# Optimization experiments

Hardware: AMD Instinct MI355X
Metric: run time of the kernel (lower is better)

The kernel has to match this reference:

```python
import jax, jax.numpy as jnp
import numpy as np

NM, ND = 50000, 50000          # mirna / disease node counts
DM, DD = 256, 256              # m_sim / d_sim feature dims
F = 64                         # feature_attn_size
E = 1600000                    # number of edges (avg degree 16)
N = NM + ND
SLOPE = 0.2                    # leaky_relu negative slope


def setup_inputs() -> dict:
    key = jax.random.key(0)
    k1, k2, k3, k4, k5, k6 = jax.random.split(key, 6)
    return {
        "m_sim": jax.random.normal(k1, (NM, DM), dtype=jnp.float32),
        "d_sim": jax.random.normal(k2, (ND, DD), dtype=jnp.float32),
        "Wm": jax.random.normal(k3, (F, DM), dtype=jnp.float32) / np.sqrt(DM).astype(np.float32),
        "Wd": jax.random.normal(k4, (F, DD), dtype=jnp.float32) / np.sqrt(DD).astype(np.float32),
        "src": jax.random.randint(k5, (E,), 0, N),
        "dst": jax.random.randint(k6, (E,), 0, N),
    }


def reference(m_sim, d_sim, Wm, Wd, src, dst):
    # node projection (dropout omitted: eval mode). mirna nodes first, then disease nodes.
    z = jnp.concatenate([m_sim @ Wm.T, d_sim @ Wd.T], axis=0)  # [N, F]

    # edge attention score: dot(z_src, z_dst) then leaky_relu
    z_src = z[src]                                             # [E, F] gather
    e = jnp.sum(z_src * z[dst], axis=1)                        # [E]
    e = jax.nn.leaky_relu(e, SLOPE)

    # segment softmax over incoming edges of each dst node (numerically stable)
    emax = jax.ops.segment_max(e, dst, num_segments=N)         # [N]
    emax = jnp.where(jnp.isfinite(emax), emax, 0.0)            # isolated nodes
    ex = jnp.exp(e - emax[dst])                                # [E]
    denom = jax.ops.segment_sum(ex, dst, num_segments=N)       # [N]
    alpha = ex / denom[dst]                                    # [E]

    # weighted aggregation + elu (isolated nodes get h=0, elu(0)=0)
    h = jax.ops.segment_sum(alpha[:, None] * z_src, dst, num_segments=N)  # [N, F]
    return jax.nn.elu(h)
```

## Files before the change

### kernel.cpp

```cpp
#include <hip/hip_runtime.h>
#include <math.h>

#define NM 50000
#define ND 50000
#define NN 100000
#define DK 256
#define F  64
#define SLOPE 0.2f

#define NBZ   391
#define NPROJ (NBZ * 2)

#define NBUCK 391
#define BCAP  8192
#define CH    4096

typedef short bf16x8 __attribute__((ext_vector_type(8)));
typedef float f32x4  __attribute__((ext_vector_type(4)));

__device__ __forceinline__ void cvt8(const float4& a0, const float4& a1,
                                     bf16x8& hi, bf16x8& lo) {
    float v[8] = {a0.x, a0.y, a0.z, a0.w, a1.x, a1.y, a1.z, a1.w};
    #pragma unroll
    for (int e = 0; e < 8; ++e) {
        unsigned u  = __float_as_uint(v[e]);
        unsigned r  = u + 0x7FFF + ((u >> 16) & 1);
        unsigned short hb = (unsigned short)(r >> 16);
        float hf = __uint_as_float(((unsigned)hb) << 16);
        float lf = v[e] - hf;
        unsigned ul = __float_as_uint(lf);
        unsigned rl = ul + 0x7FFF + ((ul >> 16) & 1);
        hi[e] = (short)hb;
        lo[e] = (short)(rl >> 16);
    }
}

__global__ __launch_bounds__(512, 1) void fused1(const float* __restrict__ m_sim,
                                                 const float* __restrict__ d_sim,
                                                 const float* __restrict__ Wm,
                                                 const float* __restrict__ Wd,
                                                 float* __restrict__ z,
                                                 const int* __restrict__ src,
                                                 const int* __restrict__ dst,
                                                 int* __restrict__ pkb_g,
                                                 int* __restrict__ bcur,
                                                 int nchunks, int E) {
    __shared__ __align__(16) char smem[65536];
    int t = threadIdx.x;

    if ((int)blockIdx.x < nchunks) {
        int* cnt   = (int*)smem;
        int* scx   = cnt + 512;
        int* lcur  = scx + 512;
        int* gbase = lcur + 512;
        int* pkb_l = gbase + 512;
        int* bkt_l = pkb_l + CH;

        int base = blockIdx.x * CH;
        int chunkN = E - base; if (chunkN > CH) chunkN = CH;

        cnt[t] = 0;
        __syncthreads();

        int ss[8], ds[8];
        #pragma unroll
        for (int e = 0; e < 8; ++e) {
            int k = base + e * 512 + t;
            if (e * 512 + t < chunkN) {
                ds[e] = dst[k];
                ss[e] = src[k];
                atomicAdd(&cnt[ds[e] >> 8], 1);
            }
        }
        __syncthreads();

        int x = cnt[t];
        scx[t] = x;
        __syncthreads();
        for (int off = 1; off < 512; off <<= 1) {
            int v = (t >= off) ? scx[t - off] : 0;
            __syncthreads();
            scx[t] += v;
            __syncthreads();
        }
        int lexcl = scx[t] - x;
        scx[t] = lexcl;
        lcur[t] = lexcl;
        gbase[t] = atomicAdd(&bcur[t], x);
        __syncthreads();

        #pragma unroll
        for (int e = 0; e < 8; ++e) {
            if (e * 512 + t < chunkN) {
                int b = ds[e] >> 8;
                int p = atomicAdd(&lcur[b], 1);
                pkb_l[p] = (ss[e] << 8) | (ds[e] & 255);
                bkt_l[p] = b;
            }
        }
        __syncthreads();

        for (int idx = t; idx < chunkN; idx += 512) {
            int b = bkt_l[idx];
            int g = b * BCAP + gbase[b] + (idx - scx[b]);
            pkb_g[g] = pkb_l[idx];
        }
        return;
    }

    short* Whi = (short*)smem;
    short* Wlo = (short*)(smem + 32768);

    int bid  = blockIdx.x - nchunks;
    bool ism = bid < NBZ;
    const float* sim = ism ? m_sim : d_sim;
    const float* W   = ism ? Wm : Wd;
    int row0   = (ism ? bid : bid - NBZ) * 128;
    int nrows  = ism ? NM : ND;
    int zbase  = ism ? 0 : NM;

    int l = t & 63;
    int w = t >> 6;
    int frow = l & 15;
    int kg   = l >> 4;

    int grow = row0 + w * 16 + frow; if (grow > nrows - 1) grow = nrows - 1;
    const float4* ap = (const float4*)(sim + (size_t)grow * DK) + kg * 2;

    float4 pa0 = ap[0], pa1 = ap[1];
    float4 pb0 = ap[8], pb1 = ap[9];

    {
        int r = t >> 3;
        int q = t & 7;
        const float4* wr = (const float4*)(W + (size_t)r * DK);
        #pragma unroll
        for (int i = 0; i < 4; ++i) {
            int ls = q * 4 + i;
            float4 b0 = wr[ls * 2], b1 = wr[ls * 2 + 1];
            bf16x8 hi, lo;
            cvt8(b0, b1, hi, lo);
            int ps = ls ^ (r & 7);
            *(bf16x8*)&Whi[r * 256 + ps * 8] = hi;
            *(bf16x8*)&Wlo[r * 256 + ps * 8] = lo;
        }
    }
    __syncthreads();

    f32x4 acc[4];
    #pragma unroll
    for (int j = 0; j < 4; ++j) acc[j] = (f32x4){0.f, 0.f, 0.f, 0.f};

    #pragma unroll 1
    for (int step = 0; step < 8; ++step) {
        bf16x8 ahi, alo;
        cvt8(pa0, pa1, ahi, alo);
        pa0 = pb0; pa1 = pb1;
        if (step + 2 < 8) {
            pb0 = ap[(step + 2) * 8];
            pb1 = ap[(step + 2) * 8 + 1];
        }

        int ls = step * 4 + kg;
        #pragma unroll
        for (int j = 0; j < 4; ++j) {
            int wrow = j * 16 + frow;
            int ps = ls ^ (wrow & 7);
            bf16x8 bhi = *(const bf16x8*)&Whi[wrow * 256 + ps * 8];
            bf16x8 blo = *(const bf16x8*)&Wlo[wrow * 256 + ps * 8];
            acc[j] = __builtin_amdgcn_mfma_f32_16x16x32_bf16(ahi, bhi, acc[j], 0, 0, 0);
            acc[j] = __builtin_amdgcn_mfma_f32_16x16x32_bf16(ahi, blo, acc[j], 0, 0, 0);
            acc[j] = __builtin_amdgcn_mfma_f32_16x16x32_bf16(alo, bhi, acc[j], 0, 0, 0);
        }
    }

    #pragma unroll
    for (int j = 0; j < 4; ++j) {
        #pragma unroll
        for (int reg = 0; reg < 4; ++reg) {
            int r = row0 + w * 16 + kg * 4 + reg;
            if (r < nrows)
                z[(size_t)(zbase + r) * F + j * 16 + frow] = acc[j][reg];
        }
    }
}

__global__ __launch_bounds__(512) void scanBuck(const int* __restrict__ bcur,
                                                int* __restrict__ bbase) {
    __shared__ int sd[512];
    int t = threadIdx.x;
    int x = (t < NBUCK) ? bcur[t] : 0;
    sd[t] = x;
    __syncthreads();
    for (int off = 1; off < 512; off <<= 1) {
        int v = (t >= off) ? sd[t - off] : 0;
        __syncthreads();
        sd[t] += v;
        __syncthreads();
    }
    if (t < NBUCK) bbase[t] = sd[t] - x;
}

__global__ __launch_bounds__(256) void scatter3(const int* __restrict__ pkb_g,
                                                const int* __restrict__ bcur,
                                                const int* __restrict__ bbase,
                                                int* __restrict__ offs,
                                                int* __restrict__ csr) {
    __shared__ int dcnt[256], loc[256], lcur[256];
    int b = blockIdx.x;
    int t = threadIdx.x;
    int node0 = b << 8;
    int nbe  = bcur[b];
    int base = bbase[b];
    const int* pp = pkb_g + (size_t)b * BCAP;

    dcnt[t] = 0;
    __syncthreads();
    for (int i = t; i < nbe; i += 256)
        atomicAdd(&dcnt[pp[i] & 255], 1);
    __syncthreads();

    int x = dcnt[t];
    loc[t] = x;
    __syncthreads();
    for (int off = 1; off < 256; off <<= 1) {
        int v = (t >= off) ? loc[t - off] : 0;
        __syncthreads();
        loc[t] += v;
        __syncthreads();
    }
    int excl = loc[t] - x;
    int node = node0 + t;
    if (node < NN) offs[node] = base + excl;
    if (b == NBUCK - 1 && t == 0) offs[NN] = base + nbe;
    lcur[t] = base + excl;
    __syncthreads();

    for (int i = t; i < nbe; i += 256) {
        int pk = pp[i];
        int pos = atomicAdd(&lcur[pk & 255], 1);
        csr[pos] = pk >> 8;
    }
}

__global__ __launch_bounds__(256) void gat_kernel(const float* __restrict__ z,
                                                  const int* __restrict__ offs,
                                                  const int* __restrict__ csr_src,
                                                  float* __restrict__ out) {
    int tid  = threadIdx.x;
    int node = blockIdx.x * 4 + (tid >> 6);
    int lane = tid & 63;
    int g    = lane >> 4;
    int i    = lane & 15;
    int beg = offs[node];
    int end = offs[node + 1];

    float4 zd = *(const float4*)&z[(size_t)node * F + i * 4];

    float  m = -1e30f, ssum = 0.f;
    float4 h = {0.f, 0.f, 0.f, 0.f};

    for (int j = beg; j < end; j += 16) {
        int   idx[4];
        bool  val[4];
        float4 v[4];
        float p[4], e[4], ex[4];
        #pragma unroll
        for (int k = 0; k < 4; ++k) {
            int jj = j + k * 4 + g;
            val[k] = jj < end;
            idx[k] = csr_src[val[k] ? jj : beg];
        }
        #pragma unroll
        for (int k = 0; k < 4; ++k)
            v[k] = *(const float4*)&z[(size_t)idx[k] * F + i * 4];
        #pragma unroll
        for (int k = 0; k < 4; ++k)
            p[k] = v[k].x * zd.x + v[k].y * zd.y + v[k].z * zd.z + v[k].w * zd.w;
        #pragma unroll
        for (int o = 1; o < 16; o <<= 1) {
            #pragma unroll
            for (int k = 0; k < 4; ++k) p[k] += __shfl_xor(p[k], o, 64);
        }
        #pragma unroll
        for (int k = 0; k < 4; ++k) {
            float ek = (p[k] > 0.f) ? p[k] : SLOPE * p[k];
            e[k] = val[k] ? ek : -1e30f;
        }
        float nm = fmaxf(m, fmaxf(fmaxf(e[0], e[1]), fmaxf(e[2], e[3])));
        float sc = __expf(m - nm);
        #pragma unroll
        for (int k = 0; k < 4; ++k) ex[k] = val[k] ? __expf(e[k] - nm) : 0.f;
        ssum = ssum * sc + ex[0] + ex[1] + ex[2] + ex[3];
        h.x = h.x * sc + ex[0] * v[0].x + ex[1] * v[1].x + ex[2] * v[2].x + ex[3] * v[3].x;
        h.y = h.y * sc + ex[0] * v[0].y + ex[1] * v[1].y + ex[2] * v[2].y + ex[3] * v[3].y;
        h.z = h.z * sc + ex[0] * v[0].z + ex[1] * v[1].z + ex[2] * v[2].z + ex[3] * v[3].z;
        h.w = h.w * sc + ex[0] * v[0].w + ex[1] * v[1].w + ex[2] * v[2].w + ex[3] * v[3].w;
        m = nm;
    }

    float M = fmaxf(m, __shfl_xor(m, 16, 64));
    M = fmaxf(M, __shfl_xor(M, 32, 64));
    float sc = __expf(m - M);
    float ss = ssum * sc;
    ss += __shfl_xor(ss, 16, 64);
    ss += __shfl_xor(ss, 32, 64);
    h.x *= sc; h.y *= sc; h.z *= sc; h.w *= sc;
    h.x += __shfl_xor(h.x, 16, 64); h.x += __shfl_xor(h.x, 32, 64);
    h.y += __shfl_xor(h.y, 16, 64); h.y += __shfl_xor(h.y, 32, 64);
    h.z += __shfl_xor(h.z, 16, 64); h.z += __shfl_xor(h.z, 32, 64);
    h.w += __shfl_xor(h.w, 16, 64); h.w += __shfl_xor(h.w, 32, 64);

    if (g == 0) {
        float rs = 1.0f / ss;
        bool has = end > beg;
        float4 o;
        o.x = has ? h.x * rs : 0.f;
        o.y = has ? h.y * rs : 0.f;
        o.z = has ? h.z * rs : 0.f;
        o.w = has ? h.w * rs : 0.f;
        o.x = (o.x > 0.f) ? o.x : (__expf(o.x) - 1.f);
        o.y = (o.y > 0.f) ? o.y : (__expf(o.y) - 1.f);
        o.z = (o.z > 0.f) ? o.z : (__expf(o.z) - 1.f);
        o.w = (o.w > 0.f) ? o.w : (__expf(o.w) - 1.f);
        *(float4*)&out[(size_t)node * F + i * 4] = o;
    }
}

extern "C" void kernel_launch(void* const* d_in, const int* in_sizes, int n_in,
                              void* d_out, int out_size, void* d_ws, size_t ws_size,
                              hipStream_t stream) {
    const float* m_sim = (const float*)d_in[0];
    const float* d_sim = (const float*)d_in[1];
    const float* Wm    = (const float*)d_in[2];
    const float* Wd    = (const float*)d_in[3];
    const int*   src   = (const int*)d_in[4];
    const int*   dst   = (const int*)d_in[5];
    int E = in_sizes[4];
    float* out = (float*)d_out;

    char* ws = (char*)d_ws;
    float* z      = (float*)ws; ws += (size_t)NN * F * 4;
    int*   offs   = (int*)ws;   ws += (size_t)(NN + 1) * 4;
    int*   bbase  = (int*)ws;   ws += 512 * 4;
    int*   bcur   = (int*)ws;   ws += 512 * 4;
    int*   csr    = (int*)ws;   ws += (size_t)E * 4;
    int*   pkb_g  = (int*)ws;   ws += (size_t)NBUCK * BCAP * 4;

    hipMemsetAsync(bcur, 0, 512 * 4, stream);

    int nchunks = (E + CH - 1) / CH;
    fused1<<<nchunks + NPROJ, 512, 0, stream>>>(m_sim, d_sim, Wm, Wd, z,
                                                src, dst, pkb_g, bcur, nchunks, E);
    scanBuck<<<1, 512, 0, stream>>>(bcur, bbase);
    scatter3<<<NBUCK, 256, 0, stream>>>(pkb_g, bcur, bbase, offs, csr);
    gat_kernel<<<NN / 4, 256, 0, stream>>>(z, offs, csr, out);
}
```

Baseline: 129.0 us.

## Fuse CSR build into GAT kernel using per-block LDS bucket sort

```diff
diff --git a/kernel.cpp b/kernel.cpp
--- a/kernel.cpp
+++ b/kernel.cpp
@@ -14,6 +14,7 @@
 #define NBUCK 391
 #define BCAP  8192
 #define CH    4096
+#define QCAP  2048
 
 typedef short bf16x8 __attribute__((ext_vector_type(8)));
 typedef float f32x4  __attribute__((ext_vector_type(4)));
@@ -180,150 +181,133 @@
         for (int reg = 0; reg < 4; ++reg) {
             int r = row0 + w * 16 + kg * 4 + reg;
             if (r < nrows)
-                z[(size_t)(zbase + r) * F + j * 16 + frow] = acc[j][reg];
+                z[((zbase + r) << 6) + j * 16 + frow] = acc[j][reg];
         }
     }
 }
 
-__global__ __launch_bounds__(512) void scanBuck(const int* __restrict__ bcur,
-                                                int* __restrict__ bbase) {
-    __shared__ int sd[512];
-    int t = threadIdx.x;
-    int x = (t < NBUCK) ? bcur[t] : 0;
-    sd[t] = x;
-    __syncthreads();
-    for (int off = 1; off < 512; off <<= 1) {
-        int v = (t >= off) ? sd[t - off] : 0;
-        __syncthreads();
-        sd[t] += v;
-        __syncthreads();
-    }
-    if (t < NBUCK) bbase[t] = sd[t] - x;
-}
-
-__global__ __launch_bounds__(256) void scatter3(const int* __restrict__ pkb_g,
-                                                const int* __restrict__ bcur,
-                                                const int* __restrict__ bbase,
-                                                int* __restrict__ offs,
-                                                int* __restrict__ csr) {
-    __shared__ int dcnt[256], loc[256], lcur[256];
-    int b = blockIdx.x;
-    int t = threadIdx.x;
-    int node0 = b << 8;
-    int nbe  = bcur[b];
-    int base = bbase[b];
+__global__ __launch_bounds__(256) void gat2(const float* __restrict__ z,
+                                            const int* __restrict__ pkb_g,
+                                            const int* __restrict__ bcur,
+                                            float* __restrict__ out) {
+    __shared__ int dcnt[64], loc[64], lcur[64];
+    __shared__ int csr_l[QCAP];
+
+    int t  = threadIdx.x;
+    int b  = blockIdx.x >> 2;
+    int q  = blockIdx.x & 3;
+    int node0 = (b << 8) + (q << 6);
+    int nbe = bcur[b];
     const int* pp = pkb_g + (size_t)b * BCAP;
 
-    dcnt[t] = 0;
-    __syncthreads();
-    for (int i = t; i < nbe; i += 256)
-        atomicAdd(&dcnt[pp[i] & 255], 1);
-    __syncthreads();
-
-    int x = dcnt[t];
-    loc[t] = x;
-    __syncthreads();
-    for (int off = 1; off < 256; off <<= 1) {
-        int v = (t >= off) ? loc[t - off] : 0;
-        __syncthreads();
-        loc[t] += v;
-        __syncthreads();
-    }
-    int excl = loc[t] - x;
-    int node = node0 + t;
-    if (node < NN) offs[node] = base + excl;
-    if (b == NBUCK - 1 && t == 0) offs[NN] = base + nbe;
-    lcur[t] = base + excl;
-    __syncthreads();
-
+    if (t < 64) dcnt[t] = 0;
+    __syncthreads();
     for (int i = t; i < nbe; i += 256) {
         int pk = pp[i];
-        int pos = atomicAdd(&lcur[pk & 255], 1);
-        csr[pos] = pk >> 8;
-    }
-}
-
-__global__ __launch_bounds__(256) void gat_kernel(const float* __restrict__ z,
-                                                  const int* __restrict__ offs,
-                                                  const int* __restrict__ csr_src,
-                                                  float* __restrict__ out) {
-    int tid  = threadIdx.x;
-    int node = blockIdx.x * 4 + (tid >> 6);
-    int lane = tid & 63;
+        if (((pk >> 6) & 3) == q) atomicAdd(&dcnt[pk & 63], 1);
+    }
+    __syncthreads();
+    if (t < 64) loc[t] = dcnt[t];
+    __syncthreads();
+    for (int off = 1; off < 64; off <<= 1) {
+        int v = (t < 64 && t >= off) ? loc[t - off] : 0;
+        __syncthreads();
+        if (t < 64) loc[t] += v;
+        __syncthreads();
+    }
+    if (t < 64) { int e0 = loc[t] - dcnt[t]; loc[t] = e0; lcur[t] = e0; }
+    __syncthreads();
+    for (int i = t; i < nbe; i += 256) {
+        int pk = pp[i];
+        if (((pk >> 6) & 3) == q) {
+            int pos = atomicAdd(&lcur[pk & 63], 1);
+            csr_l[pos] = pk >> 8;
+        }
+    }
+    __syncthreads();
+
+    int lane = t & 63;
+    int w    = t >> 6;
     int g    = lane >> 4;
-    int i    = lane & 15;
-    int beg = offs[node];
-    int end = offs[node + 1];
-
-    float4 zd = *(const float4*)&z[(size_t)node * F + i * 4];
-
-    float  m = -1e30f, ssum = 0.f;
-    float4 h = {0.f, 0.f, 0.f, 0.f};
-
-    for (int j = beg; j < end; j += 16) {
-        int   idx[4];
-        bool  val[4];
-        float4 v[4];
-        float p[4], e[4], ex[4];
-        #pragma unroll
-        for (int k = 0; k < 4; ++k) {
-            int jj = j + k * 4 + g;
-            val[k] = jj < end;
-            idx[k] = csr_src[val[k] ? jj : beg];
-        }
-        #pragma unroll
-        for (int k = 0; k < 4; ++k)
-            v[k] = *(const float4*)&z[(size_t)idx[k] * F + i * 4];
-        #pragma unroll
-        for (int k = 0; k < 4; ++k)
-            p[k] = v[k].x * zd.x + v[k].y * zd.y + v[k].z * zd.z + v[k].w * zd.w;
-        #pragma unroll
-        for (int o = 1; o < 16; o <<= 1) {
-            #pragma unroll
-            for (int k = 0; k < 4; ++k) p[k] += __shfl_xor(p[k], o, 64);
-        }
-        #pragma unroll
-        for (int k = 0; k < 4; ++k) {
-            float ek = (p[k] > 0.f) ? p[k] : SLOPE * p[k];
-            e[k] = val[k] ? ek : -1e30f;
-        }
-        float nm = fmaxf(m, fmaxf(fmaxf(e[0], e[1]), fmaxf(e[2], e[3])));
-        float sc = __expf(m - nm);
-        #pragma unroll
-        for (int k = 0; k < 4; ++k) ex[k] = val[k] ? __expf(e[k] - nm) : 0.f;
-        ssum = ssum * sc + ex[0] + ex[1] + ex[2] + ex[3];
-        h.x = h.x * sc + ex[0] * v[0].x + ex[1] * v[1].x + ex[2] * v[2].x + ex[3] * v[3].x;
-        h.y = h.y * sc + ex[0] * v[0].y + ex[1] * v[1].y + ex[2] * v[2].y + ex[3] * v[3].y;
-        h.z = h.z * sc + ex[0] * v[0].z + ex[1] * v[1].z + ex[2] * v[2].z + ex[3] * v[3].z;
-        h.w = h.w * sc + ex[0] * v[0].w + ex[1] * v[1].w + ex[2] * v[2].w + ex[3] * v[3].w;
-        m = nm;
-    }
-
-    float M = fmaxf(m, __shfl_xor(m, 16, 64));
-    M = fmaxf(M, __shfl_xor(M, 32, 64));
-    float sc = __expf(m - M);
-    float ss = ssum * sc;
-    ss += __shfl_xor(ss, 16, 64);
-    ss += __shfl_xor(ss, 32, 64);
-    h.x *= sc; h.y *= sc; h.z *= sc; h.w *= sc;
-    h.x += __shfl_xor(h.x, 16, 64); h.x += __shfl_xor(h.x, 32, 64);
-    h.y += __shfl_xor(h.y, 16, 64); h.y += __shfl_xor(h.y, 32, 64);
-    h.z += __shfl_xor(h.z, 16, 64); h.z += __shfl_xor(h.z, 32, 64);
-    h.w += __shfl_xor(h.w, 16, 64); h.w += __shfl_xor(h.w, 32, 64);
-
-    if (g == 0) {
-        float rs = 1.0f / ss;
-        bool has = end > beg;
-        float4 o;
-        o.x = has ? h.x * rs : 0.f;
-        o.y = has ? h.y * rs : 0.f;
-        o.z = has ? h.z * rs : 0.f;
-        o.w = has ? h.w * rs : 0.f;
-        o.x = (o.x > 0.f) ? o.x : (__expf(o.x) - 1.f);
-        o.y = (o.y > 0.f) ? o.y : (__expf(o.y) - 1.f);
-        o.z = (o.z > 0.f) ? o.z : (__expf(o.z) - 1.f);
-        o.w = (o.w > 0.f) ? o.w : (__expf(o.w) - 1.f);
-        *(float4*)&out[(size_t)node * F + i * 4] = o;
+    int i4   = lane & 15;
+    int iq   = i4 << 2;
+
+    for (int nn_ = 0; nn_ < 16; ++nn_) {
+        int n    = w * 16 + nn_;
+        int node = node0 + n;
+        if (node >= NN) break;
+        int beg = loc[n];
+        int end = beg + dcnt[n];
+
+        float4 zd = *(const float4*)(z + (node << 6) + iq);
+        float  m = -1e30f, ssum = 0.f;
+        float4 h = {0.f, 0.f, 0.f, 0.f};
+
+        for (int j = beg; j < end; j += 16) {
+            int   off_[4];
+            bool  val[4];
+            float4 v[4];
+            float p[4], e[4], ex[4];
+            #pragma unroll
+            for (int k = 0; k < 4; ++k) {
+                int jj = j + k * 4 + g;
+                val[k] = jj < end;
+                off_[k] = (csr_l[val[k] ? jj : beg] << 6) + iq;
+            }
+            #pragma unroll
+            for (int k = 0; k < 4; ++k)
+                v[k] = *(const float4*)(z + off_[k]);
+            #pragma unroll
+            for (int k = 0; k < 4; ++k)
+                p[k] = v[k].x * zd.x + v[k].y * zd.y + v[k].z * zd.z + v[k].w * zd.w;
+            #pragma unroll
+            for (int o = 1; o < 16; o <<= 1) {
+                #pragma unroll
+                for (int k = 0; k < 4; ++k) p[k] += __shfl_xor(p[k], o, 64);
+            }
+            #pragma unroll
+            for (int k = 0; k < 4; ++k) {
+                float ek = (p[k] > 0.f) ? p[k] : SLOPE * p[k];
+                e[k] = val[k] ? ek : -1e30f;
+            }
+            float nm = fmaxf(m, fmaxf(fmaxf(e[0], e[1]), fmaxf(e[2], e[3])));
+            float sc = __expf(m - nm);
+            #pragma unroll
+            for (int k = 0; k < 4; ++k) ex[k] = val[k] ? __expf(e[k] - nm) : 0.f;
+            ssum = ssum * sc + ex[0] + ex[1] + ex[2] + ex[3];
+            h.x = h.x * sc + ex[0] * v[0].x + ex[1] * v[1].x + ex[2] * v[2].x + ex[3] * v[3].x;
+            h.y = h.y * sc + ex[0] * v[0].y + ex[1] * v[1].y + ex[2] * v[2].y + ex[3] * v[3].y;
+            h.z = h.z * sc + ex[0] * v[0].z + ex[1] * v[1].z + ex[2] * v[2].z + ex[3] * v[3].z;
+            h.w = h.w * sc + ex[0] * v[0].w + ex[1] * v[1].w + ex[2] * v[2].w + ex[3] * v[3].w;
+            m = nm;
+        }
+
+        float M = fmaxf(m, __shfl_xor(m, 16, 64));
+        M = fmaxf(M, __shfl_xor(M, 32, 64));
+        float sc = __expf(m - M);
+        float ss = ssum * sc;
+        ss += __shfl_xor(ss, 16, 64);
+        ss += __shfl_xor(ss, 32, 64);
+        h.x *= sc; h.y *= sc; h.z *= sc; h.w *= sc;
+        h.x += __shfl_xor(h.x, 16, 64); h.x += __shfl_xor(h.x, 32, 64);
+        h.y += __shfl_xor(h.y, 16, 64); h.y += __shfl_xor(h.y, 32, 64);
+        h.z += __shfl_xor(h.z, 16, 64); h.z += __shfl_xor(h.z, 32, 64);
+        h.w += __shfl_xor(h.w, 16, 64); h.w += __shfl_xor(h.w, 32, 64);
+
+        if (g == 0) {
+            float rs = 1.0f / ss;
+            bool has = end > beg;
+            float4 o;
+            o.x = has ? h.x * rs : 0.f;
+            o.y = has ? h.y * rs : 0.f;
+            o.z = has ? h.z * rs : 0.f;
+            o.w = has ? h.w * rs : 0.f;
+            o.x = (o.x > 0.f) ? o.x : (__expf(o.x) - 1.f);
+            o.y = (o.y > 0.f) ? o.y : (__expf(o.y) - 1.f);
+            o.z = (o.z > 0.f) ? o.z : (__expf(o.z) - 1.f);
+            o.w = (o.w > 0.f) ? o.w : (__expf(o.w) - 1.f);
+            *(float4*)(out + (node << 6) + iq) = o;
+        }
     }
 }
 
@@ -341,10 +325,7 @@
 
     char* ws = (char*)d_ws;
     float* z      = (float*)ws; ws += (size_t)NN * F * 4;
-    int*   offs   = (int*)ws;   ws += (size_t)(NN + 1) * 4;
-    int*   bbase  = (int*)ws;   ws += 512 * 4;
     int*   bcur   = (int*)ws;   ws += 512 * 4;
-    int*   csr    = (int*)ws;   ws += (size_t)E * 4;
     int*   pkb_g  = (int*)ws;   ws += (size_t)NBUCK * BCAP * 4;
 
     hipMemsetAsync(bcur, 0, 512 * 4, stream);
@@ -352,7 +333,5 @@
     int nchunks = (E + CH - 1) / CH;
     fused1<<<nchunks + NPROJ, 512, 0, stream>>>(m_sim, d_sim, Wm, Wd, z,
                                                 src, dst, pkb_g, bcur, nchunks, E);
-    scanBuck<<<1, 512, 0, stream>>>(bcur, bbase);
-    scatter3<<<NBUCK, 256, 0, stream>>>(pkb_g, bcur, bbase, offs, csr);
-    gat_kernel<<<NN / 4, 256, 0, stream>>>(z, offs, csr, out);
+    gat2<<<NBUCK * 4, 256, 0, stream>>>(z, pkb_g, bcur, out);
 }
```

Result: faster. 125.1 us (-3.1%).
